# Kernel optimization log

Hardware: AMD Instinct MI355X
Metric: run time of the kernel (lower is better)

Reference implementation:

```python
import jax, jax.numpy as jnp
import numpy as np

ALPHA = 0.1  # GCN2Conv alpha; theta=None => beta=1.0 so out = ((1-a)*prop + a*x0) @ W


def gcn_norm(edge_index, n):
    # PyG gcn_norm with add_self_loops=True and unit edge weights.
    row, col = edge_index[0], edge_index[1]
    loop = jnp.arange(n, dtype=edge_index.dtype)
    row = jnp.concatenate([row, loop])
    col = jnp.concatenate([col, loop])
    w = jnp.ones(row.shape[0], dtype=jnp.float32)
    deg = jax.ops.segment_sum(w, col, num_segments=n)
    dis = jnp.where(deg > 0, jax.lax.rsqrt(jnp.maximum(deg, 1e-12)), 0.0)
    norm = dis[row] * w * dis[col]
    return row, col, norm


def propagate(x, row, col, norm, n):
    # out[col] += norm * x[row]  (source->target aggregation)
    return jax.ops.segment_sum(x[row] * norm[:, None], col, num_segments=n)


def setup_inputs() -> dict:
    key = jax.random.key(0)
    ks = jax.random.split(key, 6)
    N, E, F, L = 100000, 1000000, 64, 4
    x = jax.random.normal(ks[0], (N, F), dtype=jnp.float32)
    edge_index = jax.random.randint(ks[1], (2, E), 0, N, dtype=jnp.int64)
    gcn2_w = jax.random.normal(ks[2], (L, F, F), dtype=jnp.float32) * (1.0 / np.sqrt(F))
    w1 = jax.random.normal(ks[3], (F, 16), dtype=jnp.float32) * (1.0 / np.sqrt(F))
    b1 = jnp.zeros((16,), dtype=jnp.float32)
    w2 = jax.random.normal(ks[4], (16, 1), dtype=jnp.float32) * (1.0 / np.sqrt(16))
    b2 = jnp.zeros((1,), dtype=jnp.float32)
    return {"x": x, "edge_index": edge_index, "gcn2_w": gcn2_w,
            "w1": w1, "b1": b1, "w2": w2, "b2": b2}


def reference(x, edge_index, gcn2_w, w1, b1, w2, b2):
    n = x.shape[0]
    row, col, norm = gcn_norm(edge_index, n)
    x0 = x
    h = x
    # GCN2Conv stack: h = relu(((1-a)*Ah + a*x0) @ W)
    for l in range(gcn2_w.shape[0]):
        p = propagate(h, row, col, norm, n)
        h = jax.nn.relu(((1.0 - ALPHA) * p + ALPHA * x0) @ gcn2_w[l])
    # GCNConv(F,16): lin -> propagate -> bias
    h = propagate(h @ w1, row, col, norm, n) + b1
    # GCNConv(16,1)
    h = propagate(h @ w2, row, col, norm, n) + b2
    return jax.nn.sigmoid(h).squeeze(1).astype(jnp.float32)
```

## Files before the change

### kernel.cpp

```cpp
#include <hip/hip_runtime.h>
#include <hip/hip_fp16.h>
#include <math.h>

#define ALPHA 0.1f
#define CHUNK 8192

typedef _Float16 f16x8 __attribute__((ext_vector_type(8)));
typedef float f32x4 __attribute__((ext_vector_type(4)));


__global__ void k_zero(int* a, int n) {
    int i = blockIdx.x * blockDim.x + threadIdx.x;
    if (i < n) a[i] = 0;
}

__global__ __launch_bounds__(256) void kb_hist(const int* __restrict__ col, int e,
                                               int nbuck, int* __restrict__ tot) {
    __shared__ int h[1024];
    int t = threadIdx.x;
    for (int i = t; i < 1024; i += 256) h[i] = 0;
    __syncthreads();
    int base = blockIdx.x * CHUNK;
    int end = min(base + CHUNK, e);
    for (int i = base + t; i < end; i += 256)
        atomicAdd(&h[col[i] >> 7], 1);
    __syncthreads();
    for (int i = t; i < nbuck; i += 256)
        if (h[i]) atomicAdd(&tot[i], h[i]);
}

__global__ __launch_bounds__(1024) void kb_scan(const int* __restrict__ tot,
                                                int* __restrict__ start,
                                                int* __restrict__ cursor, int nbuck) {
    __shared__ int s[1024];
    int t = threadIdx.x;
    int v = (t < nbuck) ? tot[t] : 0;
    s[t] = v;
    __syncthreads();
    for (int d = 1; d < 1024; d <<= 1) {
        int add = (t >= d) ? s[t - d] : 0;
        __syncthreads();
        s[t] += add;
        __syncthreads();
    }
    if (t < nbuck) { start[t] = s[t] - v; cursor[t] = s[t] - v; }
    if (t == nbuck - 1) start[nbuck] = s[t];
}

__global__ __launch_bounds__(256) void kb_part(const int* __restrict__ row,
                                               const int* __restrict__ col,
                                               int e, int nbuck,
                                               int* __restrict__ cursor,
                                               int* __restrict__ part) {
    __shared__ int lcnt[1024];
    __shared__ int lbase[1024];
    int t = threadIdx.x;
    for (int i = t; i < 1024; i += 256) lcnt[i] = 0;
    __syncthreads();
    int base = blockIdx.x * CHUNK;
    int end = min(base + CHUNK, e);
    for (int i = base + t; i < end; i += 256)
        atomicAdd(&lcnt[col[i] >> 7], 1);
    __syncthreads();
    for (int i = t; i < nbuck; i += 256) {
        int c = lcnt[i];
        lbase[i] = c ? atomicAdd(&cursor[i], c) : 0;
    }
    __syncthreads();
    for (int i = t; i < 1024; i += 256) lcnt[i] = 0;
    __syncthreads();
    for (int i = base + t; i < end; i += 256) {
        int cl = col[i];
        int b = cl >> 7;
        int lp = atomicAdd(&lcnt[b], 1);
        part[lbase[b] + lp] = ((cl & 127) << 17) | row[i];
    }
}

__global__ __launch_bounds__(256) void kb_csr(const int* __restrict__ start,
                                              const int* __restrict__ part, int n,
                                              const float* __restrict__ x,
                                              float* __restrict__ dis,
                                              int* __restrict__ off,
                                              int* __restrict__ srow,
                                              __half* __restrict__ xs,
                                              __half* __restrict__ x0h) {
    __shared__ int cnt[128], excl[128], stmp[128];
    __shared__ float disl[128];
    int b = blockIdx.x;
    int t = threadIdx.x;
    int bstart = start[b], bend = start[b + 1];
    if (t < 128) cnt[t] = 0;
    __syncthreads();
    for (int i = bstart + t; i < bend; i += 256)
        atomicAdd(&cnt[part[i] >> 17], 1);
    __syncthreads();
    if (t < 128) stmp[t] = cnt[t];
    __syncthreads();
    for (int d = 1; d < 128; d <<= 1) {
        int add = (t < 128 && t >= d) ? stmp[t - d] : 0;
        __syncthreads();
        if (t < 128) stmp[t] += add;
        __syncthreads();
    }
    if (t < 128) {
        excl[t] = stmp[t] - cnt[t];
        int c = (b << 7) + t;
        float d = rsqrtf((float)cnt[t] + 1.0f);
        disl[t] = d;
        if (c < n) {
            off[c] = bstart + stmp[t];
            dis[c] = d;
        }
        cnt[t] = 0;
    }
    __syncthreads();
    for (int i = bstart + t; i < bend; i += 256) {
        int pk = part[i];
        int cl = pk >> 17;
        int lp = atomicAdd(&cnt[cl], 1);
        srow[bstart + excl[cl] + lp] = pk & 0x1FFFF;
    }
    int c0 = b << 7;
    for (int i = t; i < 128 * 64; i += 256) {
        int node = c0 + (i >> 6);
        if (node >= n) break;
        float xv = x[(size_t)node * 64 + (i & 63)];
        float d = disl[i >> 6];
        xs[(size_t)node * 64 + (i & 63)] = __float2half(d * xv);
        x0h[(size_t)node * 64 + (i & 63)] = __float2half(ALPHA * xv);
    }
}


__global__ void k_prep(const float* __restrict__ gw, const float* __restrict__ w1,
                       __half* __restrict__ whT, __half* __restrict__ w1T, int L) {
    int i = blockIdx.x * blockDim.x + threadIdx.x;
    int tot = L * 4096;
    if (i < tot) {
        int l = i >> 12, r = i & 4095;
        int k = r >> 6, nf = r & 63;
        whT[(l << 12) + nf * 64 + k] = __float2half(gw[i]);
    } else if (i < tot + 1024) {
        int r = i - tot;
        int k = r >> 4, nf = r & 15;
        w1T[nf * 64 + k] = __float2half(w1[r]);
    }
}


__global__ __launch_bounds__(256) void k_gcn2_fused(
    const int* __restrict__ srow, const int* __restrict__ endoff,
    const float* __restrict__ dis, const __half* __restrict__ hs_in,
    const __half* __restrict__ x0h, const __half* __restrict__ whT,
    __half* __restrict__ hs_out,
    const __half* __restrict__ w1T,
    __half* __restrict__ t16s, int n)
{
    __shared__ __half vs[32][72];
    __shared__ __half vs2[32][72];
    __shared__ float dcs[32];

    int t = threadIdx.x;
    int w = t >> 6;
    int lane = t & 63;
    int nb = blockIdx.x * 32;

    int j = lane >> 3;
    int s = lane & 7;
    int local = w * 8 + j;
    int c = nb + local;
    bool valid = c < n;
    int cc = valid ? c : 0;
    int start = (cc == 0) ? 0 : endoff[cc - 1];
    int end = valid ? endoff[cc] : 0;
    float dc = dis[cc];

    float a0, a1, a2, a3, a4, a5, a6, a7;
    float b0 = 0, b1 = 0, b2 = 0, b3 = 0, b4 = 0, b5 = 0, b6 = 0, b7 = 0;
    {
        f16x8 q = *(const f16x8*)(hs_in + (size_t)cc * 64 + s * 8);
        a0 = (float)q[0]; a1 = (float)q[1]; a2 = (float)q[2]; a3 = (float)q[3];
        a4 = (float)q[4]; a5 = (float)q[5]; a6 = (float)q[6]; a7 = (float)q[7];
    }
    int e = start;
    for (; e + 2 <= end; e += 2) {
        int r0 = srow[e];
        int r1 = srow[e + 1];
        f16x8 q0 = *(const f16x8*)(hs_in + (size_t)r0 * 64 + s * 8);
        f16x8 q1 = *(const f16x8*)(hs_in + (size_t)r1 * 64 + s * 8);
        a0 += (float)q0[0]; a1 += (float)q0[1]; a2 += (float)q0[2]; a3 += (float)q0[3];
        a4 += (float)q0[4]; a5 += (float)q0[5]; a6 += (float)q0[6]; a7 += (float)q0[7];
        b0 += (float)q1[0]; b1 += (float)q1[1]; b2 += (float)q1[2]; b3 += (float)q1[3];
        b4 += (float)q1[4]; b5 += (float)q1[5]; b6 += (float)q1[6]; b7 += (float)q1[7];
    }
    if (e < end) {
        int r0 = srow[e];
        f16x8 q0 = *(const f16x8*)(hs_in + (size_t)r0 * 64 + s * 8);
        a0 += (float)q0[0]; a1 += (float)q0[1]; a2 += (float)q0[2]; a3 += (float)q0[3];
        a4 += (float)q0[4]; a5 += (float)q0[5]; a6 += (float)q0[6]; a7 += (float)q0[7];
    }
    a0 += b0; a1 += b1; a2 += b2; a3 += b3;
    a4 += b4; a5 += b5; a6 += b6; a7 += b7;

    if (valid) {
        float dc9 = (1.0f - ALPHA) * dc;
        const f16x8* xp = (const f16x8*)(x0h + (size_t)cc * 64 + s * 8);
        f16x8 xv = __builtin_nontemporal_load(xp);
        f16x8 vv;
        vv[0] = (_Float16)(dc9 * a0 + (float)xv[0]);
        vv[1] = (_Float16)(dc9 * a1 + (float)xv[1]);
        vv[2] = (_Float16)(dc9 * a2 + (float)xv[2]);
        vv[3] = (_Float16)(dc9 * a3 + (float)xv[3]);
        vv[4] = (_Float16)(dc9 * a4 + (float)xv[4]);
        vv[5] = (_Float16)(dc9 * a5 + (float)xv[5]);
        vv[6] = (_Float16)(dc9 * a6 + (float)xv[6]);
        vv[7] = (_Float16)(dc9 * a7 + (float)xv[7]);
        *(f16x8*)&vs[local][s * 8] = vv;
        if (s == 0) dcs[local] = dc;
    }
    __syncthreads();

    int m16 = lane & 15;
    int quad = lane >> 4;
    f16x8 bf0 = *(const f16x8*)(whT + (size_t)(w * 16 + m16) * 64 + quad * 8);
    f16x8 bf1 = *(const f16x8*)(whT + (size_t)(w * 16 + m16) * 64 + 32 + quad * 8);
    bool last = (w1T != nullptr);
#pragma unroll
    for (int mt = 0; mt < 2; mt++) {
        f32x4 acc = {0.0f, 0.0f, 0.0f, 0.0f};
        f16x8 af0 = *(const f16x8*)&vs[mt * 16 + m16][quad * 8];
        f16x8 af1 = *(const f16x8*)&vs[mt * 16 + m16][32 + quad * 8];
        acc = __builtin_amdgcn_mfma_f32_16x16x32_f16(af0, bf0, acc, 0, 0, 0);
        acc = __builtin_amdgcn_mfma_f32_16x16x32_f16(af1, bf1, acc, 0, 0, 0);
        if (!last) {
#pragma unroll
            for (int r = 0; r < 4; r++) {
                int loc = mt * 16 + quad * 4 + r;
                int cn = nb + loc;
                if (cn < n) {
                    float h = fmaxf(acc[r], 0.0f);
                    hs_out[(size_t)cn * 64 + w * 16 + m16] = __float2half(dcs[loc] * h);
                }
            }
        } else {
#pragma unroll
            for (int r = 0; r < 4; r++) {
                int loc = mt * 16 + quad * 4 + r;
                vs2[loc][w * 16 + m16] = __float2half(fmaxf(acc[r], 0.0f));
            }
        }
    }

    if (last) {
        __syncthreads();
        if (w < 2) {
            f16x8 c0 = *(const f16x8*)(w1T + (size_t)m16 * 64 + quad * 8);
            f16x8 c1 = *(const f16x8*)(w1T + (size_t)m16 * 64 + 32 + quad * 8);
            f16x8 af0 = *(const f16x8*)&vs2[w * 16 + m16][quad * 8];
            f16x8 af1 = *(const f16x8*)&vs2[w * 16 + m16][32 + quad * 8];
            f32x4 acc = {0.0f, 0.0f, 0.0f, 0.0f};
            acc = __builtin_amdgcn_mfma_f32_16x16x32_f16(af0, c0, acc, 0, 0, 0);
            acc = __builtin_amdgcn_mfma_f32_16x16x32_f16(af1, c1, acc, 0, 0, 0);
#pragma unroll
            for (int r = 0; r < 4; r++) {
                int loc = w * 16 + quad * 4 + r;
                int cn = nb + loc;
                if (cn < n)
                    t16s[(size_t)cn * 16 + m16] = __float2half(dcs[loc] * acc[r]);
            }
        }
    }
}


__global__ __launch_bounds__(256) void k_prop16_lin2(
    const int* __restrict__ srow, const int* __restrict__ endoff,
    const float* __restrict__ dis, const __half* __restrict__ t16s,
    const float* __restrict__ b1, const float* __restrict__ w2,
    float* __restrict__ t1s, int n)
{
    int t = threadIdx.x;
    int w = t >> 6, lane = t & 63;
    int g = lane >> 2;
    int s = lane & 3;
    int c = blockIdx.x * 4 + w;
    if (c >= n) return;
    int start = (c == 0) ? 0 : endoff[c - 1];
    int end = endoff[c];
    float a0 = 0, a1 = 0, a2 = 0, a3 = 0;
    if (g == 0) {
        float2 q = *(const float2*)(t16s + (size_t)c * 16 + s * 4);
        float2 u;
        u = __half22float2(*(__half2*)&q.x); a0 = u.x; a1 = u.y;
        u = __half22float2(*(__half2*)&q.y); a2 = u.x; a3 = u.y;
    }
    for (int e = start + g; e < end; e += 16) {
        int r = srow[e];
        float2 q = *(const float2*)(t16s + (size_t)r * 16 + s * 4);
        float2 u;
        u = __half22float2(*(__half2*)&q.x); a0 += u.x; a1 += u.y;
        u = __half22float2(*(__half2*)&q.y); a2 += u.x; a3 += u.y;
    }
#pragma unroll
    for (int d = 4; d <= 32; d <<= 1) {
        a0 += __shfl_xor(a0, d, 64); a1 += __shfl_xor(a1, d, 64);
        a2 += __shfl_xor(a2, d, 64); a3 += __shfl_xor(a3, d, 64);
    }
    float dc = dis[c];
    float4 b = *(const float4*)(b1 + s * 4);
    float4 ww = *(const float4*)(w2 + s * 4);
    float partial = (dc * a0 + b.x) * ww.x + (dc * a1 + b.y) * ww.y +
                    (dc * a2 + b.z) * ww.z + (dc * a3 + b.w) * ww.w;
    partial += __shfl_xor(partial, 1, 64);
    partial += __shfl_xor(partial, 2, 64);
    if (lane == 0) t1s[c] = dc * partial;
}


__global__ void k_prop1(const int* __restrict__ srow, const int* __restrict__ endoff,
                        const float* __restrict__ dis, const float* __restrict__ t1s,
                        const float* __restrict__ b2, float* __restrict__ out, int n) {
    int c = blockIdx.x * blockDim.x + threadIdx.x;
    if (c >= n) return;
    int start = (c == 0) ? 0 : endoff[c - 1];
    int end = endoff[c];
    float ssum = t1s[c];
    for (int e = start; e < end; e++) ssum += t1s[srow[e]];
    float v = dis[c] * ssum + b2[0];
    out[c] = 1.0f / (1.0f + expf(-v));
}


static inline char* align16(char* p) {
    return (char*)(((uintptr_t)p + 15) & ~(uintptr_t)15);
}

extern "C" void kernel_launch(void* const* d_in, const int* in_sizes, int n_in,
                              void* d_out, int out_size, void* d_ws, size_t ws_size,
                              hipStream_t stream) {
    const float* x  = (const float*)d_in[0];
    const int*   ei = (const int*)d_in[1];
    const float* gw = (const float*)d_in[2];
    const float* w1 = (const float*)d_in[3];
    const float* b1 = (const float*)d_in[4];
    const float* w2 = (const float*)d_in[5];
    const float* b2 = (const float*)d_in[6];
    float* out = (float*)d_out;

    const int N = in_sizes[0] / 64;
    const int E = in_sizes[1] / 2;
    const int L = in_sizes[2] / (64 * 64);

    const int* row = ei;
    const int* col = ei + E;

    const int NB = (N + 127) >> 7;

    char* p = (char*)d_ws;
    int* off = (int*)p;            p = align16(p + (size_t)N * 4);
    float* dis = (float*)p;        p = align16(p + (size_t)N * 4);
    int* srow = (int*)p;           p = align16(p + (size_t)E * 4);
    int* bstart = (int*)p;         p = align16(p + (size_t)(NB + 1) * 4);
    int* bcur = (int*)p;           p = align16(p + (size_t)NB * 4);
    int* btot = (int*)p;           p = align16(p + (size_t)NB * 4);
    __half* whT = (__half*)p;      p = align16(p + (size_t)L * 4096 * 2);
    __half* w1T = (__half*)p;      p = align16(p + 1024 * 2);
    __half* hsA = (__half*)p;      p = align16(p + (size_t)N * 128);
    __half* hsB = (__half*)p;      p = align16(p + (size_t)N * 128);
    __half* x0h = (__half*)p;      p = align16(p + (size_t)N * 128);
    __half* t16s = (__half*)p;     p = align16(p + (size_t)N * 32);
    float* t1s = (float*)p;
    int* part = (int*)hsB;

    const int B = 256;
    int gN = (N + B - 1) / B;
    int gPart = (E + CHUNK - 1) / CHUNK;

    k_prep<<<(L * 4096 + 1024 + B - 1) / B, B, 0, stream>>>(gw, w1, whT, w1T, L);

    k_zero<<<(NB + B - 1) / B, B, 0, stream>>>(btot, NB);
    kb_hist<<<gPart, B, 0, stream>>>(col, E, NB, btot);
    kb_scan<<<1, 1024, 0, stream>>>(btot, bstart, bcur, NB);
    kb_part<<<gPart, B, 0, stream>>>(row, col, E, NB, bcur, part);
    kb_csr<<<NB, B, 0, stream>>>(bstart, part, N, x, dis, off, srow, hsA, x0h);

    __half* bufs[2] = {hsA, hsB};
    const __half* hin = hsA;
    for (int l = 0; l < L; l++) {
        bool lastl = (l == L - 1);
        __half* hout = lastl ? nullptr : bufs[(l + 1) & 1];
        k_gcn2_fused<<<(N + 31) / 32, B, 0, stream>>>(
            srow, off, dis, hin, x0h, whT + (size_t)l * 4096,
            hout, lastl ? w1T : nullptr, t16s, N);
        hin = hout;
    }

    k_prop16_lin2<<<(N + 3) / 4, B, 0, stream>>>(srow, off, dis, t16s, b1, w2, t1s, N);
    k_prop1<<<gN, B, 0, stream>>>(srow, off, dis, t1s, b2, out, N);
}
```

Measured before the change: 338.7 us.

## Split GCN2 layer into feature-sliced gather and separate MFMA GEMM kernel

Stores the hidden features in a feature-sliced layout of four 16-column slices, each 32 bytes per node. The fused gather+GEMM kernel is split into a gather kernel and a GEMM kernel. The gather kernel processes one slice per block and interleaves slices and node halves across the grid, so each slice table (about 3.2MB) can stay in L2/cache during the random neighbor gathers. This cuts wasted cache-line traffic, at the cost of an extra kernel launch per layer, an intermediate buffer write/read, and 4x more index reads of srow.

New measurement: 487.9 us. 44.0% more time.

```diff
diff --git a/kernel.cpp b/kernel.cpp
--- a/kernel.cpp
+++ b/kernel.cpp
@@ -6,7 +6,12 @@
 #define CHUNK 8192
 
 typedef _Float16 f16x8 __attribute__((ext_vector_type(8)));
+typedef _Float16 f16x2 __attribute__((ext_vector_type(2)));
 typedef float f32x4 __attribute__((ext_vector_type(4)));
+
+static __device__ __forceinline__ void nt_store_half(__half* p, float v) {
+    __builtin_nontemporal_store((_Float16)v, (_Float16*)p);
+}
 
 
 __global__ void k_zero(int* a, int n) {
@@ -78,7 +83,7 @@
 }
 
 __global__ __launch_bounds__(256) void kb_csr(const int* __restrict__ start,
-                                              const int* __restrict__ part, int n,
+                                              const int* __restrict__ part, int n, int nr,
                                               const float* __restrict__ x,
                                               float* __restrict__ dis,
                                               int* __restrict__ off,
@@ -125,10 +130,11 @@
     for (int i = t; i < 128 * 64; i += 256) {
         int node = c0 + (i >> 6);
         if (node >= n) break;
-        float xv = x[(size_t)node * 64 + (i & 63)];
+        int f = i & 63;
+        float xv = x[(size_t)node * 64 + f];
         float d = disl[i >> 6];
-        xs[(size_t)node * 64 + (i & 63)] = __float2half(d * xv);
-        x0h[(size_t)node * 64 + (i & 63)] = __float2half(ALPHA * xv);
+        xs[(size_t)(f >> 4) * nr * 16 + (size_t)node * 16 + (f & 15)] = __float2half(d * xv);
+        x0h[(size_t)node * 64 + f] = __float2half(ALPHA * xv);
     }
 }
 
@@ -149,98 +155,98 @@
 }
 
 
-__global__ __launch_bounds__(256) void k_gcn2_fused(
+__global__ __launch_bounds__(256) void k_gather_slice(
     const int* __restrict__ srow, const int* __restrict__ endoff,
-    const float* __restrict__ dis, const __half* __restrict__ hs_in,
-    const __half* __restrict__ x0h, const __half* __restrict__ whT,
-    __half* __restrict__ hs_out,
-    const __half* __restrict__ w1T,
-    __half* __restrict__ t16s, int n)
+    const float* __restrict__ dis, const __half* __restrict__ hsS,
+    const __half* __restrict__ x0h, __half* __restrict__ vS,
+    int n, int nr, int n2)
 {
-    __shared__ __half vs[32][72];
-    __shared__ __half vs2[32][72];
-    __shared__ float dcs[32];
-
-    int t = threadIdx.x;
-    int w = t >> 6;
-    int lane = t & 63;
-    int nb = blockIdx.x * 32;
-
+    int bid = blockIdx.x;
+    int pr = bid & 7;
+    int s = pr & 3;
+    int h = pr >> 2;
+    int grp = bid >> 3;
+    int t = threadIdx.x;
+    int w = t >> 6, lane = t & 63;
     int j = lane >> 3;
-    int s = lane & 7;
-    int local = w * 8 + j;
-    int c = nb + local;
-    bool valid = c < n;
-    int cc = valid ? c : 0;
-    int start = (cc == 0) ? 0 : endoff[cc - 1];
-    int end = valid ? endoff[cc] : 0;
-    float dc = dis[cc];
-
-    float a0, a1, a2, a3, a4, a5, a6, a7;
-    float b0 = 0, b1 = 0, b2 = 0, b3 = 0, b4 = 0, b5 = 0, b6 = 0, b7 = 0;
-    {
-        f16x8 q = *(const f16x8*)(hs_in + (size_t)cc * 64 + s * 8);
-        a0 = (float)q[0]; a1 = (float)q[1]; a2 = (float)q[2]; a3 = (float)q[3];
-        a4 = (float)q[4]; a5 = (float)q[5]; a6 = (float)q[6]; a7 = (float)q[7];
-    }
-    int e = start;
-    for (; e + 2 <= end; e += 2) {
-        int r0 = srow[e];
-        int r1 = srow[e + 1];
-        f16x8 q0 = *(const f16x8*)(hs_in + (size_t)r0 * 64 + s * 8);
-        f16x8 q1 = *(const f16x8*)(hs_in + (size_t)r1 * 64 + s * 8);
-        a0 += (float)q0[0]; a1 += (float)q0[1]; a2 += (float)q0[2]; a3 += (float)q0[3];
-        a4 += (float)q0[4]; a5 += (float)q0[5]; a6 += (float)q0[6]; a7 += (float)q0[7];
-        b0 += (float)q1[0]; b1 += (float)q1[1]; b2 += (float)q1[2]; b3 += (float)q1[3];
-        b4 += (float)q1[4]; b5 += (float)q1[5]; b6 += (float)q1[6]; b7 += (float)q1[7];
-    }
-    if (e < end) {
-        int r0 = srow[e];
-        f16x8 q0 = *(const f16x8*)(hs_in + (size_t)r0 * 64 + s * 8);
-        a0 += (float)q0[0]; a1 += (float)q0[1]; a2 += (float)q0[2]; a3 += (float)q0[3];
-        a4 += (float)q0[4]; a5 += (float)q0[5]; a6 += (float)q0[6]; a7 += (float)q0[7];
-    }
-    a0 += b0; a1 += b1; a2 += b2; a3 += b3;
-    a4 += b4; a5 += b5; a6 += b6; a7 += b7;
-
-    if (valid) {
+    int f4 = lane & 7;
+    int nlim = min((h + 1) * n2, n);
+    const __half* tab = hsS + (size_t)s * nr * 16;
+    __half* vout = vS + (size_t)s * nr * 16;
+
+#pragma unroll
+    for (int o = 0; o < 2; o++) {
+        int c = h * n2 + grp * 64 + w * 16 + o * 8 + j;
+        if (c >= nlim) continue;
+        int start = (c == 0) ? 0 : endoff[c - 1];
+        int end = endoff[c];
+        float dc = dis[c];
+        f16x2 sv = *(const f16x2*)(tab + (size_t)c * 16 + f4 * 2);
+        float a0 = (float)sv[0], a1 = (float)sv[1];
+        float b0 = 0.0f, b1 = 0.0f;
+        int e = start;
+        for (; e + 2 <= end; e += 2) {
+            int r0 = srow[e];
+            int r1 = srow[e + 1];
+            f16x2 q0 = *(const f16x2*)(tab + (size_t)r0 * 16 + f4 * 2);
+            f16x2 q1 = *(const f16x2*)(tab + (size_t)r1 * 16 + f4 * 2);
+            a0 += (float)q0[0]; a1 += (float)q0[1];
+            b0 += (float)q1[0]; b1 += (float)q1[1];
+        }
+        if (e < end) {
+            int r0 = srow[e];
+            f16x2 q0 = *(const f16x2*)(tab + (size_t)r0 * 16 + f4 * 2);
+            a0 += (float)q0[0]; a1 += (float)q0[1];
+        }
+        a0 += b0; a1 += b1;
         float dc9 = (1.0f - ALPHA) * dc;
-        const f16x8* xp = (const f16x8*)(x0h + (size_t)cc * 64 + s * 8);
-        f16x8 xv = __builtin_nontemporal_load(xp);
-        f16x8 vv;
+        f16x2 xv = __builtin_nontemporal_load(
+            (const f16x2*)(x0h + (size_t)c * 64 + s * 16 + f4 * 2));
+        f16x2 vv;
         vv[0] = (_Float16)(dc9 * a0 + (float)xv[0]);
         vv[1] = (_Float16)(dc9 * a1 + (float)xv[1]);
-        vv[2] = (_Float16)(dc9 * a2 + (float)xv[2]);
-        vv[3] = (_Float16)(dc9 * a3 + (float)xv[3]);
-        vv[4] = (_Float16)(dc9 * a4 + (float)xv[4]);
-        vv[5] = (_Float16)(dc9 * a5 + (float)xv[5]);
-        vv[6] = (_Float16)(dc9 * a6 + (float)xv[6]);
-        vv[7] = (_Float16)(dc9 * a7 + (float)xv[7]);
-        *(f16x8*)&vs[local][s * 8] = vv;
-        if (s == 0) dcs[local] = dc;
-    }
-    __syncthreads();
-
+        __builtin_nontemporal_store(vv, (f16x2*)(vout + (size_t)c * 16 + f4 * 2));
+    }
+}
+
+
+__global__ __launch_bounds__(256) void k_gemm(
+    const __half* __restrict__ vS, const __half* __restrict__ whT,
+    const float* __restrict__ dis,
+    __half* __restrict__ hsN,
+    const __half* __restrict__ w1T,
+    __half* __restrict__ t16s, int n, int nr)
+{
+    __shared__ __half vs2[32][72];
+    int t = threadIdx.x;
+    int w = t >> 6, lane = t & 63;
+    int nb = blockIdx.x * 32;
     int m16 = lane & 15;
     int quad = lane >> 4;
+
     f16x8 bf0 = *(const f16x8*)(whT + (size_t)(w * 16 + m16) * 64 + quad * 8);
     f16x8 bf1 = *(const f16x8*)(whT + (size_t)(w * 16 + m16) * 64 + 32 + quad * 8);
+
+    const __half* aBase0 = vS + (size_t)(quad >> 1) * nr * 16 + (quad & 1) * 8;
+    const __half* aBase1 = vS + (size_t)((quad >> 1) + 2) * nr * 16 + (quad & 1) * 8;
+
     bool last = (w1T != nullptr);
 #pragma unroll
     for (int mt = 0; mt < 2; mt++) {
+        int node = nb + mt * 16 + m16;
+        f16x8 af0 = *(const f16x8*)(aBase0 + (size_t)node * 16);
+        f16x8 af1 = *(const f16x8*)(aBase1 + (size_t)node * 16);
         f32x4 acc = {0.0f, 0.0f, 0.0f, 0.0f};
-        f16x8 af0 = *(const f16x8*)&vs[mt * 16 + m16][quad * 8];
-        f16x8 af1 = *(const f16x8*)&vs[mt * 16 + m16][32 + quad * 8];
         acc = __builtin_amdgcn_mfma_f32_16x16x32_f16(af0, bf0, acc, 0, 0, 0);
         acc = __builtin_amdgcn_mfma_f32_16x16x32_f16(af1, bf1, acc, 0, 0, 0);
         if (!last) {
 #pragma unroll
             for (int r = 0; r < 4; r++) {
-                int loc = mt * 16 + quad * 4 + r;
-                int cn = nb + loc;
+                int cn = nb + mt * 16 + quad * 4 + r;
                 if (cn < n) {
-                    float h = fmaxf(acc[r], 0.0f);
-                    hs_out[(size_t)cn * 64 + w * 16 + m16] = __float2half(dcs[loc] * h);
+                    float hv = fmaxf(acc[r], 0.0f);
+                    nt_store_half(hsN + (size_t)w * nr * 16 + (size_t)cn * 16 + m16,
+                                  dis[cn] * hv);
                 }
             }
         } else {
@@ -255,19 +261,18 @@
     if (last) {
         __syncthreads();
         if (w < 2) {
-            f16x8 c0 = *(const f16x8*)(w1T + (size_t)m16 * 64 + quad * 8);
-            f16x8 c1 = *(const f16x8*)(w1T + (size_t)m16 * 64 + 32 + quad * 8);
+            f16x8 w10 = *(const f16x8*)(w1T + (size_t)m16 * 64 + quad * 8);
+            f16x8 w11 = *(const f16x8*)(w1T + (size_t)m16 * 64 + 32 + quad * 8);
             f16x8 af0 = *(const f16x8*)&vs2[w * 16 + m16][quad * 8];
             f16x8 af1 = *(const f16x8*)&vs2[w * 16 + m16][32 + quad * 8];
             f32x4 acc = {0.0f, 0.0f, 0.0f, 0.0f};
-            acc = __builtin_amdgcn_mfma_f32_16x16x32_f16(af0, c0, acc, 0, 0, 0);
-            acc = __builtin_amdgcn_mfma_f32_16x16x32_f16(af1, c1, acc, 0, 0, 0);
+            acc = __builtin_amdgcn_mfma_f32_16x16x32_f16(af0, w10, acc, 0, 0, 0);
+            acc = __builtin_amdgcn_mfma_f32_16x16x32_f16(af1, w11, acc, 0, 0, 0);
 #pragma unroll
             for (int r = 0; r < 4; r++) {
-                int loc = w * 16 + quad * 4 + r;
-                int cn = nb + loc;
+                int cn = nb + w * 16 + quad * 4 + r;
                 if (cn < n)
-                    t16s[(size_t)cn * 16 + m16] = __float2half(dcs[loc] * acc[r]);
+                    nt_store_half(t16s + (size_t)cn * 16 + m16, dis[cn] * acc[r]);
             }
         }
     }
@@ -356,6 +361,8 @@
     const int* col = ei + E;
 
     const int NB = (N + 127) >> 7;
+    const int NR = (N + 31) & ~31;
+    const int N2 = (N + 1) / 2;
 
     char* p = (char*)d_ws;
     int* off = (int*)p;            p = align16(p + (size_t)N * 4);
@@ -366,16 +373,19 @@
     int* btot = (int*)p;           p = align16(p + (size_t)NB * 4);
     __half* whT = (__half*)p;      p = align16(p + (size_t)L * 4096 * 2);
     __half* w1T = (__half*)p;      p = align16(p + 1024 * 2);
-    __half* hsA = (__half*)p;      p = align16(p + (size_t)N * 128);
-    __half* hsB = (__half*)p;      p = align16(p + (size_t)N * 128);
-    __half* x0h = (__half*)p;      p = align16(p + (size_t)N * 128);
+    __half* hsA = (__half*)p;      p = align16(p + (size_t)NR * 128);
+    __half* hsB = (__half*)p;      p = align16(p + (size_t)NR * 128);
+    __half* vS  = (__half*)p;      p = align16(p + (size_t)NR * 128);
+    __half* x0h = (__half*)p;      p = align16(p + (size_t)NR * 128);
     __half* t16s = (__half*)p;     p = align16(p + (size_t)N * 32);
     float* t1s = (float*)p;
-    int* part = (int*)hsB;
+    int* part = (int*)vS;
 
     const int B = 256;
     int gN = (N + B - 1) / B;
     int gPart = (E + CHUNK - 1) / CHUNK;
+    int gGather = 8 * ((N2 + 63) / 64);
+    int gGemm = (N + 31) / 32;
 
     k_prep<<<(L * 4096 + 1024 + B - 1) / B, B, 0, stream>>>(gw, w1, whT, w1T, L);
 
@@ -383,16 +393,16 @@
     kb_hist<<<gPart, B, 0, stream>>>(col, E, NB, btot);
     kb_scan<<<1, 1024, 0, stream>>>(btot, bstart, bcur, NB);
     kb_part<<<gPart, B, 0, stream>>>(row, col, E, NB, bcur, part);
-    kb_csr<<<NB, B, 0, stream>>>(bstart, part, N, x, dis, off, srow, hsA, x0h);
+    kb_csr<<<NB, B, 0, stream>>>(bstart, part, N, NR, x, dis, off, srow, hsA, x0h);
 
     __half* bufs[2] = {hsA, hsB};
     const __half* hin = hsA;
     for (int l = 0; l < L; l++) {
         bool lastl = (l == L - 1);
         __half* hout = lastl ? nullptr : bufs[(l + 1) & 1];
-        k_gcn2_fused<<<(N + 31) / 32, B, 0, stream>>>(
-            srow, off, dis, hin, x0h, whT + (size_t)l * 4096,
-            hout, lastl ? w1T : nullptr, t16s, N);
+        k_gather_slice<<<gGather, B, 0, stream>>>(srow, off, dis, hin, x0h, vS, N, NR, N2);
+        k_gemm<<<gGemm, B, 0, stream>>>(vS, whT + (size_t)l * 4096, dis,
+                                        hout, lastl ? w1T : nullptr, t16s, N, NR);
         hin = hout;
     }
 
```
